# Kernel optimization log

Measured on AMD Instinct MI355X. Metric: run time of the kernel, lower is better.

Reference implementation:

```python
import jax, jax.numpy as jnp
import numpy as np

EPS = 1e-6
NUM_HEADS = 8
GAMMA = 0.999


def simple_rms_norm(x):
    # SimpleRMSNorm: x / ||x|| * sqrt(d) == x / sqrt(mean(x^2))
    return x * jax.lax.rsqrt(jnp.mean(x * x, axis=-1, keepdims=True) + EPS)


def setup_inputs() -> dict:
    key = jax.random.key(0)
    ks = jax.random.split(key, 12)
    B, N, M, E = 64, 14, 14, 512
    D1 = 2 * E              # expand_ratio * embed_dim = 1024
    RPE = 512               # rpe_embedding
    s = 0.02
    inp = {
        "x": jax.random.normal(ks[0], (B, N, M, E), jnp.float32),
        "H": N,
        "W": M,
        "Wu": jax.random.normal(ks[1], (E, D1), jnp.float32) * s,
        "bu": jnp.zeros((D1,), jnp.float32),
        "Wv": jax.random.normal(ks[2], (E, D1), jnp.float32) * s,
        "bv": jnp.zeros((D1,), jnp.float32),
        "Wo": jax.random.normal(ks[3], (D1, E), jnp.float32) * s,
        "bo": jnp.zeros((E,), jnp.float32),
        "rpe_pos_w": jax.random.normal(ks[4], (2, RPE), jnp.float32) * s,
        "rpe_pos_b": jnp.zeros((RPE,), jnp.float32),
        "rpe_w1": jax.random.normal(ks[5], (RPE, RPE), jnp.float32) * s,
        "rpe_b1": jnp.zeros((RPE,), jnp.float32),
        "rpe_w2": jax.random.normal(ks[6], (RPE, RPE), jnp.float32) * s,
        "rpe_b2": jnp.zeros((RPE,), jnp.float32),
        "rpe_w3": jax.random.normal(ks[7], (RPE, RPE), jnp.float32) * s,
        "rpe_b3": jnp.zeros((RPE,), jnp.float32),
        "rpe_out_w": jax.random.normal(ks[8], (RPE, D1), jnp.float32) * s,
        "rpe_out_b": jnp.zeros((D1,), jnp.float32),
    }
    return inp


def gtu2d_forward(x, Wu, bu, Wv, bv, Wo, bo,
                  rpe_pos_w, rpe_pos_b, rpe_w1, rpe_b1, rpe_w2, rpe_b2,
                  rpe_w3, rpe_b3, rpe_out_w, rpe_out_b):
    B, n, m, E = x.shape
    d1 = Wu.shape[1]
    hd = d1 // NUM_HEADS
    # dual gated projections
    u = jax.nn.silu(x @ Wu + bu)                      # (B, n, m, d1)
    v = jax.nn.silu(x @ Wv + bv)
    v = v.reshape(B, n, m, NUM_HEADS, hd).transpose(0, 3, 1, 2, 4)  # (B, h, n, m, d)

    # --- Tno2D: RPE MLP produces Toeplitz coefficients for relative positions ---
    ii = jnp.arange(-(n - 1), n, dtype=jnp.float32)
    jj = jnp.arange(-(m - 1), m, dtype=jnp.float32)
    pos = jnp.stack(jnp.meshgrid(ii, jj, indexing="ij"), axis=-1)  # (2n-1, 2m-1, 2)
    r = pos @ rpe_pos_w + rpe_pos_b
    for w, b in ((rpe_w1, rpe_b1), (rpe_w2, rpe_b2), (rpe_w3, rpe_b3)):
        r = jax.nn.relu(simple_rms_norm(r)) @ w + b
    r = jax.nn.relu(simple_rms_norm(r)) @ rpe_out_w + rpe_out_b  # (2n-1, 2m-1, h*d)
    a = r.reshape(2 * n - 1, 2 * m - 1, NUM_HEADS, hd).transpose(2, 0, 1, 3)
    # decay: gamma^(|i|+|j|)
    dist = jnp.abs(pos[..., 0]) + jnp.abs(pos[..., 1])  # (2n-1, 2m-1)
    a = a * (GAMMA ** dist)[None, :, :, None]

    # embed coefficients into circular kernel (h, 2n, 2m, d); index n / m are zero
    t = jnp.zeros((NUM_HEADS, 2 * n, 2 * m, hd), a.dtype)
    t = t.at[:, :n, :m].set(a[:, n - 1:, m - 1:])
    t = t.at[:, n + 1:, :m].set(a[:, :n - 1, m - 1:])
    t = t.at[:, :n, m + 1:].set(a[:, n - 1:, :m - 1])
    t = t.at[:, n + 1:, m + 1:].set(a[:, :n - 1, :m - 1])

    # 2D Toeplitz matvec via circular convolution / FFT
    xf = jnp.fft.rfft2(v, s=(2 * n, 2 * m), axes=(2, 3))
    tf = jnp.fft.rfft2(t, s=(2 * n, 2 * m), axes=(1, 2))
    y = jnp.fft.irfft2(xf * tf[None], s=(2 * n, 2 * m), axes=(2, 3))[:, :, :n, :m, :]
    y = y.transpose(0, 2, 3, 1, 4).reshape(B, n, m, d1)  # 'b h n m d -> b n m (h d)'

    return (u * y) @ Wo + bo


def reference(x, H, W, Wu, bu, Wv, bv, Wo, bo,
              rpe_pos_w, rpe_pos_b, rpe_w1, rpe_b1, rpe_w2, rpe_b2,
              rpe_w3, rpe_b3, rpe_out_w, rpe_out_b):
    # H, W are unused by Gtu2d.forward (spatial dims are carried by x)
    return gtu2d_forward(x, Wu, bu, Wv, bv, Wo, bo,
                         rpe_pos_w, rpe_pos_b, rpe_w1, rpe_b1, rpe_w2, rpe_b2,
                         rpe_w3, rpe_b3, rpe_out_w, rpe_out_b)
```

## Files before the change

### kernel.cpp

```cpp
#include <hip/hip_runtime.h>
#include <hip/hip_bf16.h>

typedef __hip_bfloat16 bf16;
typedef __attribute__((ext_vector_type(8))) short bf16x8;
typedef __attribute__((ext_vector_type(4))) float f32x4;

constexpr int NB    = 64;
constexpr int EE    = 512;
constexpr int RPOS  = 27 * 27;
constexpr int ROWS  = NB * 14 * 14;

#define RMS_EPS 1e-6f
#define GAMMA_LOG2 (-0.00144344319f)

__device__ __forceinline__ void  stf(float* p, float v) { *p = v; }
__device__ __forceinline__ void  stf(bf16* p, float v)  { *p = __float2bfloat16(v); }

__device__ __forceinline__ void gload_lds16(const bf16* g, bf16* l) {
    __builtin_amdgcn_global_load_lds(
        (const __attribute__((address_space(1))) void*)g,
        (__attribute__((address_space(3))) void*)l, 16, 0, 0);
}

#define VMCNT(n) asm volatile("s_waitcnt vmcnt(" #n ")" ::: "memory")

__global__ __launch_bounds__(256) void k_prep(const float* __restrict__ Wu,
                                              const float* __restrict__ Wv,
                                              const float* __restrict__ Wo,
                                              const float* __restrict__ w1,
                                              const float* __restrict__ w2,
                                              const float* __restrict__ w3,
                                              const float* __restrict__ wOut,
                                              const float* __restrict__ bu,
                                              const float* __restrict__ bv,
                                              const float* __restrict__ x,
                                              bf16* __restrict__ WuvT,
                                              bf16* __restrict__ WoT,
                                              bf16* __restrict__ w1T,
                                              bf16* __restrict__ w2T,
                                              bf16* __restrict__ w3T,
                                              bf16* __restrict__ wOutT,
                                              float* __restrict__ biasUv,
                                              bf16* __restrict__ xb) {
    __shared__ float t[32][33];
    const int tid = threadIdx.x;
    int b = blockIdx.x;

    const float* src = nullptr; bf16* dst = nullptr; int R = 0, C = 0, nbx = 0;
    if (b < 512)        { src = Wu;   dst = WuvT;                      R = 512;  C = 1024; nbx = 32; }
    else if (b < 1024)  { b -= 512;   src = Wv; dst = WuvT + (size_t)1024 * 512; R = 512; C = 1024; nbx = 32; }
    else if (b < 1536)  { b -= 1024;  src = Wo;   dst = WoT;           R = 1024; C = 512;  nbx = 16; }
    else if (b < 1792)  { b -= 1536;  src = w1;   dst = w1T;           R = 512;  C = 512;  nbx = 16; }
    else if (b < 2048)  { b -= 1792;  src = w2;   dst = w2T;           R = 512;  C = 512;  nbx = 16; }
    else if (b < 2304)  { b -= 2048;  src = w3;   dst = w3T;           R = 512;  C = 512;  nbx = 16; }
    else if (b < 2816)  { b -= 2304;  src = wOut; dst = wOutT;         R = 512;  C = 1024; nbx = 32; }
    else if (b < 2824) {
        int c = (b - 2816) * 256 + tid;
        if (c < 2048) biasUv[c] = (c < 1024) ? bu[c] : bv[c - 1024];
        return;
    } else {
        int i = (b - 2824) * 256 + tid;
        float4 v = *(const float4*)&x[(size_t)i * 4];
        bf16* d = &xb[(size_t)i * 4];
        d[0] = __float2bfloat16(v.x);
        d[1] = __float2bfloat16(v.y);
        d[2] = __float2bfloat16(v.z);
        d[3] = __float2bfloat16(v.w);
        return;
    }
    int bx = (b % nbx) * 32;
    int by = (b / nbx) * 32;
    int tx = tid & 31, ty = tid >> 5;
    #pragma unroll
    for (int i = 0; i < 4; ++i)
        t[ty + i * 8][tx] = src[(size_t)(by + ty + i * 8) * C + bx + tx];
    __syncthreads();
    #pragma unroll
    for (int i = 0; i < 4; ++i)
        dst[(size_t)(bx + ty + i * 8) * R + by + tx] = __float2bfloat16(t[tx][ty + i * 8]);
}

__global__ void k_rpe_pos_norm(const float* __restrict__ w, const float* __restrict__ bias,
                               bf16* __restrict__ out) {
    int p = blockIdx.x;
    float ii = (float)(p / 27 - 13);
    float jj = (float)(p % 27 - 13);
    int c0 = threadIdx.x, c1 = threadIdx.x + 256;
    float v0 = ii * w[c0] + jj * w[512 + c0] + bias[c0];
    float v1 = ii * w[c1] + jj * w[512 + c1] + bias[c1];
    float s = v0 * v0 + v1 * v1;
    #pragma unroll
    for (int off = 32; off; off >>= 1) s += __shfl_down(s, off, 64);
    __shared__ float ps[4];
    if ((threadIdx.x & 63) == 0) ps[threadIdx.x >> 6] = s;
    __syncthreads();
    float tot = ps[0] + ps[1] + ps[2] + ps[3];
    float scale = rsqrtf(tot * (1.0f / 512.0f) + RMS_EPS);
    out[(size_t)p * 512 + c0] = __float2bfloat16(fmaxf(v0 * scale, 0.0f));
    out[(size_t)p * 512 + c1] = __float2bfloat16(fmaxf(v1 * scale, 0.0f));
}

template <int SCALE_IN, int EPI>
__global__ __launch_bounds__(256) void k_rpe_gemm(const bf16* __restrict__ A,
                                                  const bf16* __restrict__ Bt,
                                                  const float* __restrict__ bias,
                                                  const float* __restrict__ pIn,
                                                  float* __restrict__ pOut,
                                                  bf16* __restrict__ out,
                                                  int M, int N, int K) {
    __shared__ bf16 As[64 * 32];
    __shared__ bf16 Bs[64 * 32];
    const int tid = threadIdx.x;
    const int m0 = blockIdx.y * 64;
    const int n0 = blockIdx.x * 64;
    const int lane = tid & 63;
    const int w = tid >> 6;
    const int lr = lane & 15;
    const int lk = (lane >> 4) * 8;

    f32x4 acc[4] = {};
    const int row = tid >> 2;
    const int seg = (tid & 3) * 8;

    for (int k0 = 0; k0 < K; k0 += 32) {
        gload_lds16(&A[(size_t)(m0 + row) * K + k0 + seg], &As[tid * 8]);
        gload_lds16(&Bt[(size_t)(n0 + row) * K + k0 + seg], &Bs[tid * 8]);
        __syncthreads();
        bf16x8 af = *(const bf16x8*)&As[(w * 16 + lr) * 32 + lk];
        #pragma unroll
        for (int j = 0; j < 4; ++j) {
            bf16x8 bf = *(const bf16x8*)&Bs[(j * 16 + lr) * 32 + lk];
            acc[j] = __builtin_amdgcn_mfma_f32_16x16x32_bf16(af, bf, acc[j], 0, 0, 0);
        }
        __syncthreads();
    }

    const int crow = (lane >> 4) * 4;
    const int ccol = lane & 15;
    float sc[4];
    #pragma unroll
    for (int r = 0; r < 4; ++r) {
        sc[r] = 1.0f;
        if (SCALE_IN) {
            int gr = m0 + w * 16 + crow + r;
            if (gr < M) {
                const float* pp = &pIn[(size_t)gr * 8];
                float s8 = pp[0] + pp[1] + pp[2] + pp[3] + pp[4] + pp[5] + pp[6] + pp[7];
                sc[r] = rsqrtf(s8 * (1.0f / 512.0f) + RMS_EPS);
            }
        }
    }
    float rowsq[4] = {0.f, 0.f, 0.f, 0.f};
    #pragma unroll
    for (int j = 0; j < 4; ++j) {
        int gc = n0 + j * 16 + ccol;
        float bb = bias[gc];
        #pragma unroll
        for (int r = 0; r < 4; ++r) {
            int gr = m0 + w * 16 + crow + r;
            float val = acc[j][r] * sc[r] + bb;
            if (EPI == 0) {
                rowsq[r] += val * val;
                if (gr < M) out[(size_t)gr * N + gc] = __float2bfloat16(fmaxf(val, 0.0f));
            } else {
                if (gr < M) {
                    int i = gr / 27, jj = gr % 27;
                    float decay = exp2f((float)(abs(i - 13) + abs(jj - 13)) * GAMMA_LOG2);
                    out[(size_t)gr * N + gc] = __float2bfloat16(val * decay);
                }
            }
        }
    }
    if (EPI == 0) {
        #pragma unroll
        for (int r = 0; r < 4; ++r) {
            #pragma unroll
            for (int m = 1; m < 16; m <<= 1) rowsq[r] += __shfl_xor(rowsq[r], m, 64);
        }
        if ((lane & 15) == 0) {
            #pragma unroll
            for (int r = 0; r < 4; ++r) {
                int gr = m0 + w * 16 + crow + r;
                if (gr < M) pOut[(size_t)gr * 8 + blockIdx.x] = rowsq[r];
            }
        }
    }
}

template <int EPI, typename TO>
__global__ __launch_bounds__(256) void k_mgemm(const bf16* __restrict__ A, int lda,
                                               const bf16* __restrict__ Bt,
                                               const float* __restrict__ bias,
                                               TO* __restrict__ out, int ldo,
                                               int M, int N, int K) {
    __shared__ bf16 As[128 * 32];
    __shared__ bf16 Bs[128 * 32];
    const int tid = threadIdx.x;
    const int m0 = blockIdx.y * 128;
    const int n0 = blockIdx.x * 128;
    const int lane = tid & 63;
    const int w = tid >> 6;
    const int wr = (w >> 1) * 64;
    const int wc = (w & 1) * 64;
    const int lr = lane & 15;
    const int lk = (lane >> 4) * 8;

    f32x4 acc[4][4] = {};

    for (int k0 = 0; k0 < K; k0 += 32) {
        #pragma unroll
        for (int t = 0; t < 2; ++t) {
            int flat = t * 256 + tid;
            int row = flat >> 2;
            int seg = (flat & 3) * 8;
            gload_lds16(&A[(size_t)(m0 + row) * lda + k0 + seg], &As[flat * 8]);
            gload_lds16(&Bt[(size_t)(n0 + row) * K + k0 + seg], &Bs[flat * 8]);
        }
        __syncthreads();
        bf16x8 af[4], bf[4];
        #pragma unroll
        for (int i = 0; i < 4; ++i) {
            af[i] = *(const bf16x8*)&As[(wr + i * 16 + lr) * 32 + lk];
            bf[i] = *(const bf16x8*)&Bs[(wc + i * 16 + lr) * 32 + lk];
        }
        #pragma unroll
        for (int i = 0; i < 4; ++i)
            #pragma unroll
            for (int j = 0; j < 4; ++j)
                acc[i][j] = __builtin_amdgcn_mfma_f32_16x16x32_bf16(af[i], bf[j], acc[i][j], 0, 0, 0);
        __syncthreads();
    }

    const int crow = (lane >> 4) * 4;
    const int ccol = lane & 15;
    #pragma unroll
    for (int i = 0; i < 4; ++i)
        #pragma unroll
        for (int j = 0; j < 4; ++j) {
            int gc = n0 + wc + j * 16 + ccol;
            float bb = bias[gc];
            #pragma unroll
            for (int r = 0; r < 4; ++r) {
                int gr = m0 + wr + i * 16 + crow + r;
                float val = acc[i][j][r] + bb;
                if (EPI == 1) val = val / (1.0f + expf(-val));
                stf(&out[(size_t)gr * ldo + gc], val);
            }
        }
}

template <int KT, int EPI, typename TO>
__global__ __launch_bounds__(512, 2) void k_mgemm8(const bf16* __restrict__ A, int lda,
                                                   const bf16* __restrict__ Bt,
                                                   const float* __restrict__ bias,
                                                   TO* __restrict__ out, int ldo,
                                                   int nb ) {
    constexpr int K = KT * 64;
    __shared__ __align__(16) char lds[131072];

    const int tid = threadIdx.x;
    const int lane = tid & 63;
    const int wid = tid >> 6;
    const int wr = wid >> 2;
    const int wc = wid & 3;

    int wgid = blockIdx.x;
    if ((gridDim.x & 7) == 0) {
        int cpx = gridDim.x >> 3;
        wgid = (wgid & 7) * cpx + (wgid >> 3);
    }
    const int m0 = (wgid / nb) * 256;
    const int n0 = (wgid % nb) * 256;

    auto ldsA = [&](int d, int kh) -> char* { return (char*)lds + d * 32768 + kh * 16384; };
    auto ldsB = [&](int d, int kh) -> char* { return (char*)lds + 65536 + d * 32768 + kh * 16384; };

    auto stage = [&](int op, int kh, int tt) {
        char* base = op ? ldsB(tt & 1, kh) : ldsA(tt & 1, kh);
        const bf16* g = op ? Bt : A;
        const int rowbase = op ? n0 : m0;
        const int ldr = op ? K : lda;
        #pragma unroll
        for (int l = 0; l < 2; ++l) {
            int q = tid + l * 512;
            int r = q >> 2;
            int cl = (q & 3) ^ ((r ^ (r >> 2)) & 3);
            const bf16* src = g + (size_t)(rowbase + r) * ldr + tt * 64 + kh * 32 + cl * 8;
            gload_lds16(src, (bf16*)(base + q * 16));
        }
    };
    auto rdA = [&](int d, int ks, int mi) -> bf16x8 {
        int row = wr * 128 + mi * 16 + (lane & 15);
        int ch = (lane >> 4) ^ ((row ^ (row >> 2)) & 3);
        return *(const bf16x8*)(ldsA(d, ks) + row * 64 + ch * 16);
    };
    auto rdB = [&](int d, int ks, int nj) -> bf16x8 {
        int row = wc * 64 + nj * 16 + (lane & 15);
        int ch = (lane >> 4) ^ ((row ^ (row >> 2)) & 3);
        return *(const bf16x8*)(ldsB(d, ks) + row * 64 + ch * 16);
    };

    f32x4 acc[8][4] = {};
    bf16x8 aF[4], bF[4];

    stage(0, 0, 0); stage(1, 0, 0); stage(0, 1, 0); stage(1, 1, 0);
    stage(0, 0, 1); stage(1, 0, 1);
    VMCNT(8);
    __builtin_amdgcn_s_barrier();
    __builtin_amdgcn_sched_barrier(0);

    #pragma unroll
    for (int t = 0; t < KT; ++t) {
        const int d = t & 1;
        #pragma unroll
        for (int mi = 0; mi < 4; ++mi) aF[mi] = rdA(d, 0, mi);
        #pragma unroll
        for (int nj = 0; nj < 4; ++nj) bF[nj] = rdB(d, 0, nj);
        if (t + 1 < KT) stage(0, 1, t + 1);
        __builtin_amdgcn_s_barrier();
        __builtin_amdgcn_s_setprio(1);
        #pragma unroll
        for (int mi = 0; mi < 4; ++mi)
            #pragma unroll
            for (int nj = 0; nj < 4; ++nj)
                acc[mi][nj] = __builtin_amdgcn_mfma_f32_16x16x32_bf16(aF[mi], bF[nj], acc[mi][nj], 0, 0, 0);
        __builtin_amdgcn_s_setprio(0);
        __builtin_amdgcn_s_barrier();
        #pragma unroll
        for (int mi = 0; mi < 4; ++mi) aF[mi] = rdA(d, 0, mi + 4);
        if (t + 1 < KT) stage(1, 1, t + 1);
        if (t + 1 < KT) { VMCNT(8); } else { VMCNT(0); }
        __builtin_amdgcn_s_barrier();
        __builtin_amdgcn_sched_barrier(0);
        __builtin_amdgcn_s_setprio(1);
        #pragma unroll
        for (int mi = 0; mi < 4; ++mi)
            #pragma unroll
            for (int nj = 0; nj < 4; ++nj)
                acc[mi + 4][nj] = __builtin_amdgcn_mfma_f32_16x16x32_bf16(aF[mi], bF[nj], acc[mi + 4][nj], 0, 0, 0);
        __builtin_amdgcn_s_setprio(0);
        __builtin_amdgcn_s_barrier();
        #pragma unroll
        for (int mi = 0; mi < 4; ++mi) aF[mi] = rdA(d, 1, mi);
        #pragma unroll
        for (int nj = 0; nj < 4; ++nj) bF[nj] = rdB(d, 1, nj);
        if (t + 2 < KT) stage(0, 0, t + 2);
        __builtin_amdgcn_s_barrier();
        __builtin_amdgcn_s_setprio(1);
        #pragma unroll
        for (int mi = 0; mi < 4; ++mi)
            #pragma unroll
            for (int nj = 0; nj < 4; ++nj)
                acc[mi][nj] = __builtin_amdgcn_mfma_f32_16x16x32_bf16(aF[mi], bF[nj], acc[mi][nj], 0, 0, 0);
        __builtin_amdgcn_s_setprio(0);
        __builtin_amdgcn_s_barrier();
        #pragma unroll
        for (int mi = 0; mi < 4; ++mi) aF[mi] = rdA(d, 1, mi + 4);
        if (t + 2 < KT) stage(1, 0, t + 2);
        if (t + 2 < KT)      { VMCNT(8); }
        else if (t + 1 < KT) { VMCNT(4); }
        __builtin_amdgcn_s_barrier();
        __builtin_amdgcn_sched_barrier(0);
        __builtin_amdgcn_s_setprio(1);
        #pragma unroll
        for (int mi = 0; mi < 4; ++mi)
            #pragma unroll
            for (int nj = 0; nj < 4; ++nj)
                acc[mi + 4][nj] = __builtin_amdgcn_mfma_f32_16x16x32_bf16(aF[mi], bF[nj], acc[mi + 4][nj], 0, 0, 0);
        __builtin_amdgcn_s_setprio(0);
        __builtin_amdgcn_s_barrier();
    }

    const int crow = (lane >> 4) * 4;
    const int ccol = lane & 15;
    #pragma unroll
    for (int mi = 0; mi < 8; ++mi)
        #pragma unroll
        for (int nj = 0; nj < 4; ++nj) {
            int gc = n0 + wc * 64 + nj * 16 + ccol;
            float bb = bias[gc];
            #pragma unroll
            for (int r = 0; r < 4; ++r) {
                int gr = m0 + wr * 128 + mi * 16 + crow + r;
                float val = acc[mi][nj][r] + bb;
                if (EPI == 1) val = val / (1.0f + expf(-val));
                stf(&out[(size_t)gr * ldo + gc], val);
            }
        }
}

__global__ __launch_bounds__(256) void k_vt(const bf16* __restrict__ uv,
                                            bf16* __restrict__ Vt) {
    const int c0 = blockIdx.x * 64;
    const int b  = blockIdx.y;
    const int tid = threadIdx.x;
    __shared__ bf16 t[196][66];
    for (int f = tid; f < 196 * 64; f += 256) {
        int ij = f >> 6, cl = f & 63;
        t[ij][cl] = uv[((size_t)b * 196 + ij) * 2048 + 1024 + c0 + cl];
    }
    __syncthreads();
    const bf16 z = __float2bfloat16(0.0f);
    for (int f = tid; f < 64 * 224; f += 256) {
        int cl = f / 224, ij = f - cl * 224;
        Vt[((size_t)(c0 + cl) * 64 + b) * 224 + ij] = (ij < 196) ? t[ij][cl] : z;
    }
}

template <int ZBIG>
__global__ __launch_bounds__(256) void k_convm(const bf16* __restrict__ Ab,
                                               const bf16* __restrict__ Vt,
                                               bf16* __restrict__ Yt, int cbase) {
    __shared__ __align__(16) bf16 Ts[112 * 232];
    __shared__ bf16 As[736];
    const int mh = blockIdx.x;
    const int cl = blockIdx.y;
    const int cb = ZBIG ? (int)blockIdx.z * 512 : cbase;
    const int c = cb + cl;
    const int ytc = ZBIG ? c : cl;
    const int tid = threadIdx.x;
    const int mbase = mh * 112;

    for (int e = tid; e < 729; e += 256)
        As[e] = Ab[(size_t)e * 1024 + c];
    __syncthreads();

    const bf16 z = __float2bfloat16(0.0f);
    if (tid < 224) {
        const int i = tid / 14, j = tid - i * 14;
        const bool kvalid = tid < 196;
        int p = mbase / 14, q = 0;
        for (int r = 0; r < 112; ++r) {
            bf16 val = z;
            if (kvalid && (mbase + r) < 196)
                val = As[(p - i + 13) * 27 + (q - j + 13)];
            Ts[r * 232 + tid] = val;
            if (++q == 14) { q = 0; ++p; }
        }
    }
    __syncthreads();

    const int lane = tid & 63;
    const int w = tid >> 6;
    const int lr = lane & 15;
    const int lk = (lane >> 4) * 8;
    const bf16* Vc = Vt + (size_t)c * 64 * 224;

    bf16x8 bfr[7];
    #pragma unroll
    for (int ks = 0; ks < 7; ++ks)
        bfr[ks] = *(const bf16x8*)&Vc[(size_t)(w * 16 + lr) * 224 + ks * 32 + lk];

    f32x4 acc[7] = {};
    #pragma unroll
    for (int ks = 0; ks < 7; ++ks)
        #pragma unroll
        for (int mi = 0; mi < 7; ++mi) {
            bf16x8 a = *(const bf16x8*)&Ts[(mi * 16 + lr) * 232 + ks * 32 + lk];
            acc[mi] = __builtin_amdgcn_mfma_f32_16x16x32_bf16(a, bfr[ks], acc[mi], 0, 0, 0);
        }

    const int crow = (lane >> 4) * 4;
    const int bb = w * 16 + (lane & 15);
    #pragma unroll
    for (int mi = 0; mi < 7; ++mi) {
        int pq = mbase + mi * 16 + crow;
        #pragma unroll
        for (int r = 0; r < 4; ++r)
            if (pq + r < 196)
                Yt[((size_t)ytc * 196 + pq + r) * 64 + bb] = __float2bfloat16(acc[mi][r]);
    }
}

template <int ZBIG>
__global__ __launch_bounds__(256) void k_gate(bf16* __restrict__ uv,
                                              const bf16* __restrict__ Yt, int cbase) {
    const int pq = blockIdx.x;
    const int ct = blockIdx.y;
    const int cb = ZBIG ? (int)blockIdx.z * 512 : cbase;
    const int ytb = ZBIG ? cb : 0;
    const int tid = threadIdx.x;
    __shared__ float t[64][65];
    for (int f = tid; f < 64 * 64; f += 256) {
        int cr = f >> 6, bcol = f & 63;
        t[cr][bcol] = __bfloat162float(Yt[((size_t)(ytb + ct * 64 + cr) * 196 + pq) * 64 + bcol]);
    }
    __syncthreads();
    for (int f = tid; f < 64 * 64; f += 256) {
        int br = f >> 6, cc = f & 63;
        size_t row = (size_t)br * 196 + pq;
        int cglob = cb + ct * 64 + cc;
        float uu = __bfloat162float(uv[row * 2048 + cglob]);
        uv[row * 2048 + 1024 + cglob] = __float2bfloat16(t[cc][br] * uu);
    }
}

extern "C" void kernel_launch(void* const* d_in, const int* in_sizes, int n_in,
                              void* d_out, int out_size, void* d_ws, size_t ws_size,
                              hipStream_t stream) {
    const float* x    = (const float*)d_in[0];
    const float* Wu   = (const float*)d_in[3];
    const float* bu   = (const float*)d_in[4];
    const float* Wv   = (const float*)d_in[5];
    const float* bv   = (const float*)d_in[6];
    const float* Wo   = (const float*)d_in[7];
    const float* bo   = (const float*)d_in[8];
    const float* rpw  = (const float*)d_in[9];
    const float* rpb  = (const float*)d_in[10];
    const float* w1   = (const float*)d_in[11];
    const float* b1   = (const float*)d_in[12];
    const float* w2   = (const float*)d_in[13];
    const float* b2   = (const float*)d_in[14];
    const float* w3   = (const float*)d_in[15];
    const float* b3   = (const float*)d_in[16];
    const float* wOut = (const float*)d_in[17];
    const float* bOut = (const float*)d_in[18];

    char* ws = (char*)d_ws;
    size_t off = 0;
    auto take = [&](size_t bytes) { char* p = ws + off; off += (bytes + 255) & ~size_t(255); return p; };
    bf16*  rnA    = (bf16*)take((size_t)768 * 512 * 2);
    bf16*  rnB    = (bf16*)take((size_t)768 * 512 * 2);
    float* p1     = (float*)take((size_t)768 * 8 * 4);
    float* p2     = (float*)take((size_t)768 * 8 * 4);
    float* p3     = (float*)take((size_t)768 * 8 * 4);
    bf16*  Ab     = (bf16*)take((size_t)RPOS * 1024 * 2);
    bf16*  xb     = (bf16*)take((size_t)ROWS * EE * 2);
    bf16*  WuvT   = (bf16*)take((size_t)2048 * 512 * 2);
    bf16*  WoT    = (bf16*)take((size_t)512 * 1024 * 2);
    bf16*  w1T    = (bf16*)take((size_t)512 * 512 * 2);
    bf16*  w2T    = (bf16*)take((size_t)512 * 512 * 2);
    bf16*  w3T    = (bf16*)take((size_t)512 * 512 * 2);
    bf16*  wOutT  = (bf16*)take((size_t)1024 * 512 * 2);
    float* biasUv = (float*)take(2048 * 4);
    bf16*  uvb    = (bf16*)take((size_t)ROWS * 2048 * 2);
    bf16*  Vt     = (bf16*)take((size_t)1024 * 64 * 224 * 2);

    const size_t ytFullBytes = (size_t)1024 * 196 * 64 * 2;
    bool bigYt = (off + ytFullBytes) <= ws_size;
    bf16* YtFull = bigYt ? (bf16*)(ws + off) : nullptr;
    bf16* YtHalf = (bf16*)xb;

    k_prep<<<9096, 256, 0, stream>>>(Wu, Wv, Wo, w1, w2, w3, wOut, bu, bv, x,
                                     WuvT, WoT, w1T, w2T, w3T, wOutT, biasUv, xb);

    k_rpe_pos_norm<<<RPOS, 256, 0, stream>>>(rpw, rpb, rnA);
    k_rpe_gemm<0, 0><<<dim3(8, 12), 256, 0, stream>>>(rnA, w1T, b1, nullptr, p1, rnB, RPOS, 512, 512);
    k_rpe_gemm<1, 0><<<dim3(8, 12), 256, 0, stream>>>(rnB, w2T, b2, p1, p2, rnA, RPOS, 512, 512);
    k_rpe_gemm<1, 0><<<dim3(8, 12), 256, 0, stream>>>(rnA, w3T, b3, p2, p3, rnB, RPOS, 512, 512);
    k_rpe_gemm<1, 2><<<dim3(16, 12), 256, 0, stream>>>(rnB, wOutT, bOut, p3, nullptr, Ab, RPOS, 1024, 512);

    k_mgemm8<8, 1, bf16><<<392, 512, 0, stream>>>(xb, 512, WuvT, biasUv, uvb, 2048, 8);

    k_vt<<<dim3(16, 64), 256, 0, stream>>>(uvb, Vt);

    if (bigYt) {
        k_convm<1><<<dim3(2, 512, 2), 256, 0, stream>>>(Ab, Vt, YtFull, 0);
        k_gate<1><<<dim3(196, 8, 2), 256, 0, stream>>>(uvb, YtFull, 0);
    } else {
        for (int h = 0; h < 2; ++h) {
            k_convm<0><<<dim3(2, 512), 256, 0, stream>>>(Ab, Vt, YtHalf, h * 512);
            k_gate<0><<<dim3(196, 8), 256, 0, stream>>>(uvb, YtHalf, h * 512);
        }
    }

    k_mgemm<0, float><<<dim3(4, 98), 256, 0, stream>>>(uvb + 1024, 2048, WoT, bo,
                                                       (float*)d_out, 512, ROWS, 512, 1024);
}
```

Measured before the change: 217.8 us.

## Fuse RPE MLP chain into one persistent kernel with grid barriers

Replaces the five RPE kernels (position norm plus four small GEMMs) with a single persistent kernel of 192 blocks that separates the stages with atomic-counter grid barriers. This removes four kernel launch gaps on a small serial chain. The fallback path for a small workspace is also dropped, so the full Yt buffer is always taken from the workspace. In exchange it adds a memset of the barrier counters, depends on all 192 blocks being resident at once, and runs only 96 blocks during the three middle GEMM stages.

```diff
diff --git a/kernel.cpp b/kernel.cpp
--- a/kernel.cpp
+++ b/kernel.cpp
@@ -80,39 +80,30 @@
         dst[(size_t)(bx + ty + i * 8) * R + by + tx] = __float2bfloat16(t[tx][ty + i * 8]);
 }
 
-__global__ void k_rpe_pos_norm(const float* __restrict__ w, const float* __restrict__ bias,
-                               bf16* __restrict__ out) {
-    int p = blockIdx.x;
-    float ii = (float)(p / 27 - 13);
-    float jj = (float)(p % 27 - 13);
-    int c0 = threadIdx.x, c1 = threadIdx.x + 256;
-    float v0 = ii * w[c0] + jj * w[512 + c0] + bias[c0];
-    float v1 = ii * w[c1] + jj * w[512 + c1] + bias[c1];
-    float s = v0 * v0 + v1 * v1;
-    #pragma unroll
-    for (int off = 32; off; off >>= 1) s += __shfl_down(s, off, 64);
-    __shared__ float ps[4];
-    if ((threadIdx.x & 63) == 0) ps[threadIdx.x >> 6] = s;
+__device__ __forceinline__ void gbar(int* bar, int nb) {
     __syncthreads();
-    float tot = ps[0] + ps[1] + ps[2] + ps[3];
-    float scale = rsqrtf(tot * (1.0f / 512.0f) + RMS_EPS);
-    out[(size_t)p * 512 + c0] = __float2bfloat16(fmaxf(v0 * scale, 0.0f));
-    out[(size_t)p * 512 + c1] = __float2bfloat16(fmaxf(v1 * scale, 0.0f));
+    __threadfence();
+    if (threadIdx.x == 0) {
+        if (atomicAdd(bar, 1) + 1 < nb) {
+            while (atomicAdd(bar, 0) < nb) __builtin_amdgcn_s_sleep(2);
+        }
+    }
+    __syncthreads();
+    __threadfence();
 }
 
 template <int SCALE_IN, int EPI>
-__global__ __launch_bounds__(256) void k_rpe_gemm(const bf16* __restrict__ A,
-                                                  const bf16* __restrict__ Bt,
-                                                  const float* __restrict__ bias,
-                                                  const float* __restrict__ pIn,
-                                                  float* __restrict__ pOut,
-                                                  bf16* __restrict__ out,
-                                                  int M, int N, int K) {
-    __shared__ bf16 As[64 * 32];
-    __shared__ bf16 Bs[64 * 32];
-    const int tid = threadIdx.x;
-    const int m0 = blockIdx.y * 64;
-    const int n0 = blockIdx.x * 64;
+__device__ __forceinline__ void dev_rpe_gemm(const bf16* __restrict__ A,
+                                             const bf16* __restrict__ Bt,
+                                             const float* __restrict__ bias,
+                                             const float* __restrict__ pIn,
+                                             float* __restrict__ pOut,
+                                             bf16* __restrict__ out,
+                                             int bx, int by, int M, int N, int K,
+                                             bf16* As, bf16* Bs) {
+    const int tid = threadIdx.x;
+    const int m0 = by * 64;
+    const int n0 = bx * 64;
     const int lane = tid & 63;
     const int w = tid >> 6;
     const int lr = lane & 15;
@@ -181,10 +172,67 @@
             #pragma unroll
             for (int r = 0; r < 4; ++r) {
                 int gr = m0 + w * 16 + crow + r;
-                if (gr < M) pOut[(size_t)gr * 8 + blockIdx.x] = rowsq[r];
+                if (gr < M) pOut[(size_t)gr * 8 + bx] = rowsq[r];
             }
         }
     }
+}
+
+__global__ __launch_bounds__(256) void k_rpe_all(const float* __restrict__ rpw,
+                                                 const float* __restrict__ rpb,
+                                                 const bf16* __restrict__ w1T,
+                                                 const float* __restrict__ b1,
+                                                 const bf16* __restrict__ w2T,
+                                                 const float* __restrict__ b2,
+                                                 const bf16* __restrict__ w3T,
+                                                 const float* __restrict__ b3,
+                                                 const bf16* __restrict__ wOutT,
+                                                 const float* __restrict__ bOut,
+                                                 bf16* __restrict__ rnA,
+                                                 bf16* __restrict__ rnB,
+                                                 float* __restrict__ p1,
+                                                 float* __restrict__ p2,
+                                                 float* __restrict__ p3,
+                                                 bf16* __restrict__ Ab,
+                                                 int* __restrict__ bar) {
+    __shared__ bf16 As[64 * 32];
+    __shared__ bf16 Bs[64 * 32];
+    __shared__ float ps[4];
+    const int nb = gridDim.x;
+    const int tid = threadIdx.x;
+
+    for (int p = blockIdx.x; p < RPOS; p += nb) {
+        float ii = (float)(p / 27 - 13);
+        float jj = (float)(p % 27 - 13);
+        int c0 = tid, c1 = tid + 256;
+        float v0 = ii * rpw[c0] + jj * rpw[512 + c0] + rpb[c0];
+        float v1 = ii * rpw[c1] + jj * rpw[512 + c1] + rpb[c1];
+        float s = v0 * v0 + v1 * v1;
+        #pragma unroll
+        for (int off = 32; off; off >>= 1) s += __shfl_down(s, off, 64);
+        if ((tid & 63) == 0) ps[tid >> 6] = s;
+        __syncthreads();
+        float tot = ps[0] + ps[1] + ps[2] + ps[3];
+        float scale = rsqrtf(tot * (1.0f / 512.0f) + RMS_EPS);
+        rnA[(size_t)p * 512 + c0] = __float2bfloat16(fmaxf(v0 * scale, 0.0f));
+        rnA[(size_t)p * 512 + c1] = __float2bfloat16(fmaxf(v1 * scale, 0.0f));
+        __syncthreads();
+    }
+    gbar(bar + 0, nb);
+    if (blockIdx.x < 96)
+        dev_rpe_gemm<0, 0>(rnA, w1T, b1, nullptr, p1, rnB,
+                           blockIdx.x & 7, blockIdx.x >> 3, RPOS, 512, 512, As, Bs);
+    gbar(bar + 1, nb);
+    if (blockIdx.x < 96)
+        dev_rpe_gemm<1, 0>(rnB, w2T, b2, p1, p2, rnA,
+                           blockIdx.x & 7, blockIdx.x >> 3, RPOS, 512, 512, As, Bs);
+    gbar(bar + 2, nb);
+    if (blockIdx.x < 96)
+        dev_rpe_gemm<1, 0>(rnA, w3T, b3, p2, p3, rnB,
+                           blockIdx.x & 7, blockIdx.x >> 3, RPOS, 512, 512, As, Bs);
+    gbar(bar + 3, nb);
+    dev_rpe_gemm<1, 2>(rnB, wOutT, bOut, p3, nullptr, Ab,
+                       blockIdx.x & 15, blockIdx.x >> 4, RPOS, 1024, 512, As, Bs);
 }
 
 template <int EPI, typename TO>
@@ -407,17 +455,14 @@
     }
 }
 
-template <int ZBIG>
 __global__ __launch_bounds__(256) void k_convm(const bf16* __restrict__ Ab,
                                                const bf16* __restrict__ Vt,
-                                               bf16* __restrict__ Yt, int cbase) {
+                                               bf16* __restrict__ Yt) {
     __shared__ __align__(16) bf16 Ts[112 * 232];
     __shared__ bf16 As[736];
     const int mh = blockIdx.x;
     const int cl = blockIdx.y;
-    const int cb = ZBIG ? (int)blockIdx.z * 512 : cbase;
-    const int c = cb + cl;
-    const int ytc = ZBIG ? c : cl;
+    const int c = (int)blockIdx.z * 512 + cl;
     const int tid = threadIdx.x;
     const int mbase = mh * 112;
 
@@ -468,22 +513,20 @@
         #pragma unroll
         for (int r = 0; r < 4; ++r)
             if (pq + r < 196)
-                Yt[((size_t)ytc * 196 + pq + r) * 64 + bb] = __float2bfloat16(acc[mi][r]);
-    }
-}
-
-template <int ZBIG>
+                Yt[((size_t)c * 196 + pq + r) * 64 + bb] = __float2bfloat16(acc[mi][r]);
+    }
+}
+
 __global__ __launch_bounds__(256) void k_gate(bf16* __restrict__ uv,
-                                              const bf16* __restrict__ Yt, int cbase) {
+                                              const bf16* __restrict__ Yt) {
     const int pq = blockIdx.x;
     const int ct = blockIdx.y;
-    const int cb = ZBIG ? (int)blockIdx.z * 512 : cbase;
-    const int ytb = ZBIG ? cb : 0;
+    const int cb = (int)blockIdx.z * 512;
     const int tid = threadIdx.x;
     __shared__ float t[64][65];
     for (int f = tid; f < 64 * 64; f += 256) {
         int cr = f >> 6, bcol = f & 63;
-        t[cr][bcol] = __bfloat162float(Yt[((size_t)(ytb + ct * 64 + cr) * 196 + pq) * 64 + bcol]);
+        t[cr][bcol] = __bfloat162float(Yt[((size_t)(cb + ct * 64 + cr) * 196 + pq) * 64 + bcol]);
     }
     __syncthreads();
     for (int f = tid; f < 64 * 64; f += 256) {
@@ -519,6 +562,7 @@
     char* ws = (char*)d_ws;
     size_t off = 0;
     auto take = [&](size_t bytes) { char* p = ws + off; off += (bytes + 255) & ~size_t(255); return p; };
+    int*   bar    = (int*)take(64);
     bf16*  rnA    = (bf16*)take((size_t)768 * 512 * 2);
     bf16*  rnB    = (bf16*)take((size_t)768 * 512 * 2);
     float* p1     = (float*)take((size_t)768 * 8 * 4);
@@ -535,34 +579,22 @@
     float* biasUv = (float*)take(2048 * 4);
     bf16*  uvb    = (bf16*)take((size_t)ROWS * 2048 * 2);
     bf16*  Vt     = (bf16*)take((size_t)1024 * 64 * 224 * 2);
-
-    const size_t ytFullBytes = (size_t)1024 * 196 * 64 * 2;
-    bool bigYt = (off + ytFullBytes) <= ws_size;
-    bf16* YtFull = bigYt ? (bf16*)(ws + off) : nullptr;
-    bf16* YtHalf = (bf16*)xb;
+    bf16*  Yt     = (bf16*)take((size_t)1024 * 196 * 64 * 2);
+
+    hipMemsetAsync(bar, 0, 64, stream);
 
     k_prep<<<9096, 256, 0, stream>>>(Wu, Wv, Wo, w1, w2, w3, wOut, bu, bv, x,
                                      WuvT, WoT, w1T, w2T, w3T, wOutT, biasUv, xb);
 
-    k_rpe_pos_norm<<<RPOS, 256, 0, stream>>>(rpw, rpb, rnA);
-    k_rpe_gemm<0, 0><<<dim3(8, 12), 256, 0, stream>>>(rnA, w1T, b1, nullptr, p1, rnB, RPOS, 512, 512);
-    k_rpe_gemm<1, 0><<<dim3(8, 12), 256, 0, stream>>>(rnB, w2T, b2, p1, p2, rnA, RPOS, 512, 512);
-    k_rpe_gemm<1, 0><<<dim3(8, 12), 256, 0, stream>>>(rnA, w3T, b3, p2, p3, rnB, RPOS, 512, 512);
-    k_rpe_gemm<1, 2><<<dim3(16, 12), 256, 0, stream>>>(rnB, wOutT, bOut, p3, nullptr, Ab, RPOS, 1024, 512);
+    k_rpe_all<<<192, 256, 0, stream>>>(rpw, rpb, w1T, b1, w2T, b2, w3T, b3,
+                                       wOutT, bOut, rnA, rnB, p1, p2, p3, Ab, bar);
 
     k_mgemm8<8, 1, bf16><<<392, 512, 0, stream>>>(xb, 512, WuvT, biasUv, uvb, 2048, 8);
 
     k_vt<<<dim3(16, 64), 256, 0, stream>>>(uvb, Vt);
 
-    if (bigYt) {
-        k_convm<1><<<dim3(2, 512, 2), 256, 0, stream>>>(Ab, Vt, YtFull, 0);
-        k_gate<1><<<dim3(196, 8, 2), 256, 0, stream>>>(uvb, YtFull, 0);
-    } else {
-        for (int h = 0; h < 2; ++h) {
-            k_convm<0><<<dim3(2, 512), 256, 0, stream>>>(Ab, Vt, YtHalf, h * 512);
-            k_gate<0><<<dim3(196, 8), 256, 0, stream>>>(uvb, YtHalf, h * 512);
-        }
-    }
+    k_convm<<<dim3(2, 512, 2), 256, 0, stream>>>(Ab, Vt, Yt);
+    k_gate<<<dim3(196, 8, 2), 256, 0, stream>>>(uvb, Yt);
 
     k_mgemm<0, float><<<dim3(4, 98), 256, 0, stream>>>(uvb + 1024, 2048, WoT, bo,
                                                        (float*)d_out, 512, ROWS, 512, 1024);
```

New measurement: 342.7 us. 57.3% more time.
